# Optimization experiments

Hardware: AMD Instinct MI355X
Metric: run time of the kernel (lower is better)

Reference implementation:

```python
import jax, jax.numpy as jnp
import numpy as np

N_NODES = 50000
N_EDGES = 800000
IN_FEATS = 1024
LAYERS = [128, 128]
EPS = 1e-5  # BatchNorm1d eps


def setup_inputs() -> dict:
    key = jax.random.key(0)
    ks = jax.random.split(key, 24)
    inp = {}
    inp["in_feat"] = jax.random.normal(ks[0], (N_NODES, IN_FEATS), jnp.float32)
    inp["src"] = jax.random.randint(ks[1], (N_EDGES,), 0, N_NODES, dtype=jnp.int32)
    inp["dst"] = jax.random.randint(ks[2], (N_EDGES,), 0, N_NODES, dtype=jnp.int32)
    dims = [IN_FEATS] + LAYERS
    i = 3
    for l in range(len(LAYERS)):
        din, dout = dims[l], dims[l + 1]
        s = 1.0 / np.sqrt(din)
        inp[f"W{l}"] = jax.random.uniform(ks[i], (din, dout), jnp.float32, -s, s); i += 1
        inp[f"b{l}"] = jnp.zeros((dout,), jnp.float32)
        inp[f"Wr{l}"] = jax.random.uniform(ks[i], (din, dout), jnp.float32, -s, s); i += 1
        inp[f"br{l}"] = jnp.zeros((dout,), jnp.float32)
        inp[f"gamma{l}"] = jnp.ones((dout,), jnp.float32)
        inp[f"beta{l}"] = jnp.zeros((dout,), jnp.float32)
        inp[f"mean{l}"] = jnp.zeros((dout,), jnp.float32)
        inp[f"var{l}"] = jnp.ones((dout,), jnp.float32)
    s = 1.0 / np.sqrt(LAYERS[-1])
    inp["Wd"] = jax.random.uniform(ks[i], (LAYERS[-1], 2), jnp.float32, -s, s)
    inp["bd"] = jnp.zeros((2,), jnp.float32)
    return inp


def gcn_layer(h, src, dst, W, b, Wr, br, gamma, beta, mean, var):
    # dgllife GCNLayer: GraphConv(norm='none', activation=relu) -> residual -> dropout(id, eval) -> BN(eval)
    msg = (h @ W)[src]                                        # [E, dout] gather of transformed src feats
    agg = jax.ops.segment_sum(msg, dst, num_segments=N_NODES)  # scatter-add to dst nodes
    new = jax.nn.relu(agg + b)                                 # GraphConv bias + activation
    res = jax.nn.relu(h @ Wr + br)                             # residual Linear + activation
    new = new + res
    return (new - mean) * jax.lax.rsqrt(var + EPS) * gamma + beta  # BatchNorm1d eval


def reference(in_feat, src, dst,
              W0, b0, Wr0, br0, gamma0, beta0, mean0, var0,
              W1, b1, Wr1, br1, gamma1, beta1, mean1, var1,
              Wd, bd):
    h = gcn_layer(in_feat, src, dst, W0, b0, Wr0, br0, gamma0, beta0, mean0, var0)
    h = gcn_layer(h, src, dst, W1, b1, Wr1, br1, gamma1, beta1, mean1, var1)
    logits = h @ Wd + bd                                       # [N, 2]
    return jax.nn.softmax(logits, axis=1)
```

## Files before the change

### kernel.cpp

```cpp
#include <hip/hip_runtime.h>
#include <math.h>

#define NNODES 50000
#define NEDGES 800000
#define KIN 1024
#define DH 128

typedef __bf16 bf16x8 __attribute__((ext_vector_type(8)));
typedef float floatx4 __attribute__((ext_vector_type(4)));

__global__ void k_zero2(int* __restrict__ a, int* __restrict__ b, int n) {
  int i = blockIdx.x * blockDim.x + threadIdx.x;
  if (i < n) { a[i] = 0; b[i] = 0; }
}

__global__ void k_hist(const int* __restrict__ dst, int* __restrict__ cnt, int E) {
  int i = blockIdx.x * blockDim.x + threadIdx.x;
  if (i < E) atomicAdd(&cnt[dst[i]], 1);
}

__global__ __launch_bounds__(1024) void k_scan_local(const int* __restrict__ cnt,
                                                     int* __restrict__ row_ptr,
                                                     int* __restrict__ bsum, int n) {
  __shared__ int sd[1024];
  int t = threadIdx.x;
  int i = blockIdx.x * 1024 + t;
  int v = (i < n) ? cnt[i] : 0;
  sd[t] = v;
  __syncthreads();
  for (int off = 1; off < 1024; off <<= 1) {
    int tv = (t >= off) ? sd[t - off] : 0;
    __syncthreads();
    sd[t] += tv;
    __syncthreads();
  }
  if (i < n) row_ptr[i] = sd[t] - v;
  if (t == 1023) bsum[blockIdx.x] = sd[t];
}

__global__ void k_scan_sums(const int* __restrict__ bsum, int* __restrict__ boff,
                            int nb, int* __restrict__ row_ptr, int n) {
  int lane = threadIdx.x;
  int v = (lane < nb) ? bsum[lane] : 0;
  int incl = v;
  for (int off = 1; off < 64; off <<= 1) {
    int t = __shfl_up(incl, off);
    if (lane >= off) incl += t;
  }
  boff[lane] = incl - v;
  if (lane == 63) row_ptr[n] = incl;
}

__global__ void k_scan_add(int* __restrict__ row_ptr, const int* __restrict__ boff, int n) {
  int i = blockIdx.x * blockDim.x + threadIdx.x;
  if (i < n) row_ptr[i] += boff[i >> 10];
}

__global__ void k_fill(const int* __restrict__ src, const int* __restrict__ dst,
                       const int* __restrict__ row_ptr, int* __restrict__ cursor,
                       int* __restrict__ csr_src, int E) {
  int i = blockIdx.x * blockDim.x + threadIdx.x;
  if (i < E) {
    int d = dst[i];
    int pos = row_ptr[d] + atomicAdd(&cursor[d], 1);
    csr_src[pos] = src[i];
  }
}

__global__ __launch_bounds__(256) void k_prepB(const float* __restrict__ W,
                                               const float* __restrict__ Wr,
                                               __bf16* __restrict__ Bt, int K, int kbits) {
  int id = blockIdx.x * 256 + threadIdx.x;
  int k = id & (K - 1);
  int n = id >> kbits;
  float v = (n < DH) ? W[(size_t)k * DH + n] : Wr[(size_t)k * DH + (n - DH)];
  Bt[(size_t)n * K + k] = (__bf16)v;
}

__device__ __forceinline__ void load_lds16(const void* g, void* l) {
  __builtin_amdgcn_global_load_lds(
      (const __attribute__((address_space(1))) unsigned int*)g,
      (__attribute__((address_space(3))) unsigned int*)l, 16, 0, 0);
}

template <typename AT, int K>
__global__ __launch_bounds__(256, 4) void k_gemm_mfma(
    const AT* __restrict__ X, const __bf16* __restrict__ Bt,
    const float* __restrict__ br, __bf16* __restrict__ XW,
    float* __restrict__ RES, int M) {
  __shared__ alignas(16) __bf16 As[32 * 72];
  __shared__ alignas(16) __bf16 Bs[256 * 64];
  const int tid = threadIdx.x;
  const int lane = tid & 63;
  const int w = tid >> 6;
  const int l15 = lane & 15;
  const int quad = lane >> 4;
  const int bm0 = blockIdx.x * 32;

  const int arow = tid >> 3;
  const int akq = (tid & 7) << 3;
  int agrow = bm0 + arow; if (agrow > M - 1) agrow = M - 1;
  const AT* aptr = X + (size_t)agrow * K + akq;

  floatx4 acc[2][4];
#pragma unroll
  for (int i = 0; i < 2; ++i)
#pragma unroll
    for (int j = 0; j < 4; ++j) acc[i][j] = (floatx4)0.f;

  for (int k0 = 0; k0 < K; k0 += 64) {
    if constexpr (sizeof(AT) == 4) {
      const float4 u = *(const float4*)(aptr + k0);
      const float4 v = *(const float4*)(aptr + k0 + 4);
      bf16x8 h;
      h[0] = (__bf16)u.x; h[1] = (__bf16)u.y; h[2] = (__bf16)u.z; h[3] = (__bf16)u.w;
      h[4] = (__bf16)v.x; h[5] = (__bf16)v.y; h[6] = (__bf16)v.z; h[7] = (__bf16)v.w;
      *(bf16x8*)&As[arow * 72 + akq] = h;
    } else {
      *(bf16x8*)&As[arow * 72 + akq] = *(const bf16x8*)(aptr + k0);
    }
#pragma unroll
    for (int ii = 0; ii < 8; ++ii) {
      const int wi = ii * 4 + w;
      const int n = wi * 8 + (lane >> 3);
      const int c = lane & 7;
      const int cs = c ^ (n & 7);
      const char* g = (const char*)Bt + (size_t)n * (K * 2) + (size_t)k0 * 2 + cs * 16;
      load_lds16(g, (char*)Bs + wi * 1024);
    }
    __syncthreads();
    bf16x8 af[2][2], bfr[4][2];
#pragma unroll
    for (int mt = 0; mt < 2; ++mt)
#pragma unroll
      for (int ks = 0; ks < 2; ++ks)
        af[mt][ks] = *(const bf16x8*)&As[(mt * 16 + l15) * 72 + ks * 32 + quad * 8];
#pragma unroll
    for (int nt = 0; nt < 4; ++nt) {
      const int n = w * 64 + nt * 16 + l15;
#pragma unroll
      for (int ks = 0; ks < 2; ++ks) {
        const int ch = (ks * 4 + quad) ^ (n & 7);
        bfr[nt][ks] = *(const bf16x8*)&Bs[n * 64 + ch * 8];
      }
    }
#pragma unroll
    for (int ks = 0; ks < 2; ++ks)
#pragma unroll
      for (int mt = 0; mt < 2; ++mt)
#pragma unroll
        for (int nt = 0; nt < 4; ++nt)
          acc[mt][nt] = __builtin_amdgcn_mfma_f32_16x16x32_bf16(af[mt][ks], bfr[nt][ks],
                                                                acc[mt][nt], 0, 0, 0);
    __syncthreads();
  }

  float* Cb = (float*)Bs;
#pragma unroll
  for (int mt = 0; mt < 2; ++mt)
#pragma unroll
    for (int nt = 0; nt < 4; ++nt)
#pragma unroll
      for (int r = 0; r < 4; ++r)
        Cb[(mt * 16 + quad * 4 + r) * 256 + (w * 64 + nt * 16 + l15)] = acc[mt][nt][r];
  __syncthreads();
  const int row = tid >> 3;
  const int seg = tid & 7;
  const int grow = bm0 + row;
  if (grow < M) {
    if (seg < 4) {
      const int c0 = seg * 32;
#pragma unroll
      for (int j = 0; j < 4; ++j) {
        const float4 v0 = *(const float4*)&Cb[row * 256 + c0 + j * 8];
        const float4 v1 = *(const float4*)&Cb[row * 256 + c0 + j * 8 + 4];
        bf16x8 h;
        h[0] = (__bf16)v0.x; h[1] = (__bf16)v0.y; h[2] = (__bf16)v0.z; h[3] = (__bf16)v0.w;
        h[4] = (__bf16)v1.x; h[5] = (__bf16)v1.y; h[6] = (__bf16)v1.z; h[7] = (__bf16)v1.w;
        *(bf16x8*)&XW[(size_t)grow * DH + c0 + j * 8] = h;
      }
    } else {
      const int c0 = (seg - 4) * 32;
#pragma unroll
      for (int j = 0; j < 8; ++j) {
        const float4 v = *(const float4*)&Cb[row * 256 + 128 + c0 + j * 4];
        const float4 bb = *(const float4*)&br[c0 + j * 4];
        *(float4*)&RES[(size_t)grow * DH + c0 + j * 4] =
            make_float4(fmaxf(v.x + bb.x, 0.f), fmaxf(v.y + bb.y, 0.f),
                        fmaxf(v.z + bb.z, 0.f), fmaxf(v.w + bb.w, 0.f));
      }
    }
  }
}

template <int MODE>
__global__ __launch_bounds__(256) void k_agg2(
    const __bf16* __restrict__ XW, const float* __restrict__ RES,
    const int* __restrict__ row_ptr, const int* __restrict__ csr_src,
    const float* __restrict__ b, const float* __restrict__ gamma,
    const float* __restrict__ beta, const float* __restrict__ mean,
    const float* __restrict__ var, const float* __restrict__ Wd,
    const float* __restrict__ bd, void* __restrict__ hout, int M) {
  const int node = (blockIdx.x << 2) + (threadIdx.x >> 6);
  const int lane = threadIdx.x & 63;
  if (node >= M) return;
  const int s = row_ptr[node], e = row_ptr[node + 1];
  const unsigned* xw = (const unsigned*)XW;
  float ax = 0.f, ay = 0.f;
  int i = s;
  for (; i + 3 < e; i += 4) {
    const int s0 = csr_src[i], s1 = csr_src[i + 1], s2 = csr_src[i + 2], s3 = csr_src[i + 3];
    const unsigned u0 = xw[(size_t)s0 * 64 + lane];
    const unsigned u1 = xw[(size_t)s1 * 64 + lane];
    const unsigned u2 = xw[(size_t)s2 * 64 + lane];
    const unsigned u3 = xw[(size_t)s3 * 64 + lane];
    ax += __uint_as_float(u0 << 16) + __uint_as_float(u1 << 16) +
          __uint_as_float(u2 << 16) + __uint_as_float(u3 << 16);
    ay += __uint_as_float(u0 & 0xffff0000u) + __uint_as_float(u1 & 0xffff0000u) +
          __uint_as_float(u2 & 0xffff0000u) + __uint_as_float(u3 & 0xffff0000u);
  }
  for (; i < e; ++i) {
    const unsigned u = xw[(size_t)csr_src[i] * 64 + lane];
    ax += __uint_as_float(u << 16);
    ay += __uint_as_float(u & 0xffff0000u);
  }
  const int f0 = lane << 1;
  const float2 bb = *(const float2*)&b[f0];
  const float2 rr = *(const float2*)&RES[(size_t)node * DH + f0];
  const float2 mm = *(const float2*)&mean[f0];
  const float2 vv = *(const float2*)&var[f0];
  const float2 gg = *(const float2*)&gamma[f0];
  const float2 be = *(const float2*)&beta[f0];
  const float x0 = fmaxf(ax + bb.x, 0.f) + rr.x;
  const float x1 = fmaxf(ay + bb.y, 0.f) + rr.y;
  const float y0 = (x0 - mm.x) * rsqrtf(vv.x + 1e-5f) * gg.x + be.x;
  const float y1 = (x1 - mm.y) * rsqrtf(vv.y + 1e-5f) * gg.y + be.y;
  if (MODE == 0) {
    union { __bf16 h[2]; unsigned u; } pk;
    pk.h[0] = (__bf16)y0;
    pk.h[1] = (__bf16)y1;
    ((unsigned*)hout)[(size_t)node * 64 + lane] = pk.u;
  } else {
    const float4 wv = *(const float4*)&Wd[f0 * 2];
    float l0 = y0 * wv.x + y1 * wv.z;
    float l1 = y0 * wv.y + y1 * wv.w;
#pragma unroll
    for (int off = 32; off > 0; off >>= 1) {
      l0 += __shfl_down(l0, off);
      l1 += __shfl_down(l1, off);
    }
    if (lane == 0) {
      l0 += bd[0];
      l1 += bd[1];
      const float m = fmaxf(l0, l1);
      const float e0 = expf(l0 - m), e1 = expf(l1 - m);
      const float inv = 1.f / (e0 + e1);
      float* out = (float*)hout;
      out[(size_t)node * 2] = e0 * inv;
      out[(size_t)node * 2 + 1] = e1 * inv;
    }
  }
}

extern "C" void kernel_launch(void* const* d_in, const int* in_sizes, int n_in,
                              void* d_out, int out_size, void* d_ws, size_t ws_size,
                              hipStream_t stream) {
  const float* in_feat = (const float*)d_in[0];
  const int* src = (const int*)d_in[1];
  const int* dst = (const int*)d_in[2];
  const float* W0 = (const float*)d_in[3];
  const float* b0 = (const float*)d_in[4];
  const float* Wr0 = (const float*)d_in[5];
  const float* br0 = (const float*)d_in[6];
  const float* gamma0 = (const float*)d_in[7];
  const float* beta0 = (const float*)d_in[8];
  const float* mean0 = (const float*)d_in[9];
  const float* var0 = (const float*)d_in[10];
  const float* W1 = (const float*)d_in[11];
  const float* b1 = (const float*)d_in[12];
  const float* Wr1 = (const float*)d_in[13];
  const float* br1 = (const float*)d_in[14];
  const float* gamma1 = (const float*)d_in[15];
  const float* beta1 = (const float*)d_in[16];
  const float* mean1 = (const float*)d_in[17];
  const float* var1 = (const float*)d_in[18];
  const float* Wd = (const float*)d_in[19];
  const float* bd = (const float*)d_in[20];
  float* out = (float*)d_out;

  char* ws = (char*)d_ws;
  size_t off = 0;
  auto alloc = [&](size_t bytes) {
    void* p = ws + off;
    off += (bytes + 255) & ~(size_t)255;
    return p;
  };
  __bf16* XWb = (__bf16*)alloc(sizeof(__bf16) * (size_t)NNODES * DH);
  __bf16* h1 = (__bf16*)alloc(sizeof(__bf16) * (size_t)NNODES * DH);
  float* RES = (float*)alloc(sizeof(float) * (size_t)NNODES * DH);
  int* cnt = (int*)alloc(sizeof(int) * NNODES);
  int* cursor = (int*)alloc(sizeof(int) * NNODES);
  int* row_ptr = (int*)alloc(sizeof(int) * (NNODES + 1));
  int* csr_src = (int*)alloc(sizeof(int) * NEDGES);
  int* bsum = (int*)alloc(sizeof(int) * 64);
  int* boff = (int*)alloc(sizeof(int) * 64);
  __bf16* Bt0 = (__bf16*)alloc(sizeof(__bf16) * 256 * KIN);
  __bf16* Bt1 = (__bf16*)alloc(sizeof(__bf16) * 256 * DH);

  const int nb = (NNODES + 1023) / 1024;
  k_zero2<<<(NNODES + 255) / 256, 256, 0, stream>>>(cnt, cursor, NNODES);
  k_hist<<<(NEDGES + 255) / 256, 256, 0, stream>>>(dst, cnt, NEDGES);
  k_scan_local<<<nb, 1024, 0, stream>>>(cnt, row_ptr, bsum, NNODES);
  k_scan_sums<<<1, 64, 0, stream>>>(bsum, boff, nb, row_ptr, NNODES);
  k_scan_add<<<(NNODES + 255) / 256, 256, 0, stream>>>(row_ptr, boff, NNODES);
  k_fill<<<(NEDGES + 255) / 256, 256, 0, stream>>>(src, dst, row_ptr, cursor, csr_src, NEDGES);

  k_prepB<<<KIN, 256, 0, stream>>>(W0, Wr0, Bt0, KIN, 10);
  k_prepB<<<DH, 256, 0, stream>>>(W1, Wr1, Bt1, DH, 7);

  const int ggrid = (NNODES + 31) / 32;
  const int agrid = (NNODES + 3) / 4;
  k_gemm_mfma<float, KIN><<<ggrid, 256, 0, stream>>>(in_feat, Bt0, br0, XWb, RES, NNODES);
  k_agg2<0><<<agrid, 256, 0, stream>>>(XWb, RES, row_ptr, csr_src, b0, gamma0, beta0,
                                       mean0, var0, nullptr, nullptr, h1, NNODES);
  k_gemm_mfma<__bf16, DH><<<ggrid, 256, 0, stream>>>(h1, Bt1, br1, XWb, RES, NNODES);
  k_agg2<1><<<agrid, 256, 0, stream>>>(XWb, RES, row_ptr, csr_src, b1, gamma1, beta1,
                                       mean1, var1, Wd, bd, out, NNODES);
}
```

Before: 556.2 us.

## Pre-pack weights in MFMA fragment order and stage full A tile in LDS

Weights are now packed once into the exact per-lane MFMA B-fragment layout, so the GEMM reads B straight from global/L2 into registers with coalesced 16-byte loads instead of staging it through LDS every k-step. The whole 32xK A tile is loaded and converted to bf16 in one pass into a swizzled LDS buffer, which removes the per-iteration syncthreads from the main loop. The cost is 64KB of LDS per block for K=1024, which limits occupancy, and B traffic now relies on the cache for reuse across blocks.

```diff
diff --git a/kernel.cpp b/kernel.cpp
--- a/kernel.cpp
+++ b/kernel.cpp
@@ -67,29 +67,35 @@
   }
 }
 
-__global__ __launch_bounds__(256) void k_prepB(const float* __restrict__ W,
+__global__ __launch_bounds__(256) void k_prepF(const float* __restrict__ W,
                                                const float* __restrict__ Wr,
-                                               __bf16* __restrict__ Bt, int K, int kbits) {
-  int id = blockIdx.x * 256 + threadIdx.x;
-  int k = id & (K - 1);
-  int n = id >> kbits;
-  float v = (n < DH) ? W[(size_t)k * DH + n] : Wr[(size_t)k * DH + (n - DH)];
-  Bt[(size_t)n * K + k] = (__bf16)v;
-}
-
-__device__ __forceinline__ void load_lds16(const void* g, void* l) {
-  __builtin_amdgcn_global_load_lds(
-      (const __attribute__((address_space(1))) unsigned int*)g,
-      (__attribute__((address_space(3))) unsigned int*)l, 16, 0, 0);
+                                               __bf16* __restrict__ Bf) {
+  const int id = blockIdx.x * 256 + threadIdx.x;
+  const int lane = id & 63;
+  const int ks = (id >> 6) & 1;
+  const int nt = (id >> 7) & 15;
+  const int kb = id >> 11;
+  const int n = nt * 16 + (lane & 15);
+  const int k0 = kb * 64 + ks * 32 + (lane >> 4) * 8;
+  bf16x8 h;
+#pragma unroll
+  for (int j = 0; j < 8; ++j) {
+    const int k = k0 + j;
+    const float v = (n < DH) ? W[(size_t)k * DH + n] : Wr[(size_t)k * DH + (n - DH)];
+    h[j] = (__bf16)v;
+  }
+  *(bf16x8*)&Bf[(size_t)id * 8] = h;
 }
 
 template <typename AT, int K>
-__global__ __launch_bounds__(256, 4) void k_gemm_mfma(
-    const AT* __restrict__ X, const __bf16* __restrict__ Bt,
+__global__ __launch_bounds__(256) void k_gemm3(
+    const AT* __restrict__ X, const __bf16* __restrict__ Bf,
     const float* __restrict__ br, __bf16* __restrict__ XW,
     float* __restrict__ RES, int M) {
-  __shared__ alignas(16) __bf16 As[32 * 72];
-  __shared__ alignas(16) __bf16 Bs[256 * 64];
+  constexpr unsigned ABYTES = 32u * K * 2u;
+  constexpr unsigned SMEM = (ABYTES > 32768u) ? ABYTES : 32768u;
+  __shared__ alignas(16) char smem[SMEM];
+  __bf16* As = (__bf16*)smem;
   const int tid = threadIdx.x;
   const int lane = tid & 63;
   const int w = tid >> 6;
@@ -97,10 +103,28 @@
   const int quad = lane >> 4;
   const int bm0 = blockIdx.x * 32;
 
-  const int arow = tid >> 3;
-  const int akq = (tid & 7) << 3;
-  int agrow = bm0 + arow; if (agrow > M - 1) agrow = M - 1;
-  const AT* aptr = X + (size_t)agrow * K + akq;
+  {
+    const int row = tid >> 3;
+    int grow = bm0 + row;
+    if (grow > M - 1) grow = M - 1;
+    const AT* ap = X + (size_t)grow * K;
+#pragma unroll 4
+    for (int j = 0; j < K / 64; ++j) {
+      const int c = (tid & 7) + 8 * j;
+      bf16x8 h;
+      if constexpr (sizeof(AT) == 4) {
+        const float4 u = *(const float4*)(ap + c * 8);
+        const float4 v = *(const float4*)(ap + c * 8 + 4);
+        h[0] = (__bf16)u.x; h[1] = (__bf16)u.y; h[2] = (__bf16)u.z; h[3] = (__bf16)u.w;
+        h[4] = (__bf16)v.x; h[5] = (__bf16)v.y; h[6] = (__bf16)v.z; h[7] = (__bf16)v.w;
+      } else {
+        h = *(const bf16x8*)(ap + c * 8);
+      }
+      const int cs = (c & ~7) | ((c ^ row) & 7);
+      *(bf16x8*)&As[(size_t)row * K + (cs << 3)] = h;
+    }
+  }
+  __syncthreads();
 
   floatx4 acc[2][4];
 #pragma unroll
@@ -108,42 +132,27 @@
 #pragma unroll
     for (int j = 0; j < 4; ++j) acc[i][j] = (floatx4)0.f;
 
-  for (int k0 = 0; k0 < K; k0 += 64) {
-    if constexpr (sizeof(AT) == 4) {
-      const float4 u = *(const float4*)(aptr + k0);
-      const float4 v = *(const float4*)(aptr + k0 + 4);
-      bf16x8 h;
-      h[0] = (__bf16)u.x; h[1] = (__bf16)u.y; h[2] = (__bf16)u.z; h[3] = (__bf16)u.w;
-      h[4] = (__bf16)v.x; h[5] = (__bf16)v.y; h[6] = (__bf16)v.z; h[7] = (__bf16)v.w;
-      *(bf16x8*)&As[arow * 72 + akq] = h;
-    } else {
-      *(bf16x8*)&As[arow * 72 + akq] = *(const bf16x8*)(aptr + k0);
-    }
-#pragma unroll
-    for (int ii = 0; ii < 8; ++ii) {
-      const int wi = ii * 4 + w;
-      const int n = wi * 8 + (lane >> 3);
-      const int c = lane & 7;
-      const int cs = c ^ (n & 7);
-      const char* g = (const char*)Bt + (size_t)n * (K * 2) + (size_t)k0 * 2 + cs * 16;
-      load_lds16(g, (char*)Bs + wi * 1024);
-    }
-    __syncthreads();
-    bf16x8 af[2][2], bfr[4][2];
+#pragma unroll 2
+  for (int kb = 0; kb < K / 64; ++kb) {
+    bf16x8 bfr[4][2];
+#pragma unroll
+    for (int nt = 0; nt < 4; ++nt)
+#pragma unroll
+      for (int ks = 0; ks < 2; ++ks) {
+        const int ntg = (w << 2) + nt;
+        const size_t idx = ((((size_t)kb * 16 + ntg) * 2 + ks) * 64 + lane) * 8;
+        bfr[nt][ks] = *(const bf16x8*)(Bf + idx);
+      }
+    bf16x8 af[2][2];
 #pragma unroll
     for (int mt = 0; mt < 2; ++mt)
 #pragma unroll
-      for (int ks = 0; ks < 2; ++ks)
-        af[mt][ks] = *(const bf16x8*)&As[(mt * 16 + l15) * 72 + ks * 32 + quad * 8];
-#pragma unroll
-    for (int nt = 0; nt < 4; ++nt) {
-      const int n = w * 64 + nt * 16 + l15;
-#pragma unroll
       for (int ks = 0; ks < 2; ++ks) {
-        const int ch = (ks * 4 + quad) ^ (n & 7);
-        bfr[nt][ks] = *(const bf16x8*)&Bs[n * 64 + ch * 8];
-      }
-    }
+        const int row = mt * 16 + l15;
+        const int c = kb * 8 + ks * 4 + quad;
+        const int cs = (c & ~7) | ((c ^ row) & 7);
+        af[mt][ks] = *(const bf16x8*)&As[(size_t)row * K + (cs << 3)];
+      }
 #pragma unroll
     for (int ks = 0; ks < 2; ++ks)
 #pragma unroll
@@ -152,17 +161,17 @@
         for (int nt = 0; nt < 4; ++nt)
           acc[mt][nt] = __builtin_amdgcn_mfma_f32_16x16x32_bf16(af[mt][ks], bfr[nt][ks],
                                                                 acc[mt][nt], 0, 0, 0);
-    __syncthreads();
-  }
-
-  float* Cb = (float*)Bs;
+  }
+
+  __syncthreads();
+  float* Cb = (float*)smem;
 #pragma unroll
   for (int mt = 0; mt < 2; ++mt)
 #pragma unroll
     for (int nt = 0; nt < 4; ++nt)
 #pragma unroll
       for (int r = 0; r < 4; ++r)
-        Cb[(mt * 16 + quad * 4 + r) * 256 + (w * 64 + nt * 16 + l15)] = acc[mt][nt][r];
+        Cb[(mt * 16 + quad * 4 + r) * 256 + ((w << 6) + nt * 16 + l15)] = acc[mt][nt][r];
   __syncthreads();
   const int row = tid >> 3;
   const int seg = tid & 7;
@@ -304,8 +313,8 @@
   int* csr_src = (int*)alloc(sizeof(int) * NEDGES);
   int* bsum = (int*)alloc(sizeof(int) * 64);
   int* boff = (int*)alloc(sizeof(int) * 64);
-  __bf16* Bt0 = (__bf16*)alloc(sizeof(__bf16) * 256 * KIN);
-  __bf16* Bt1 = (__bf16*)alloc(sizeof(__bf16) * 256 * DH);
+  __bf16* Bf0 = (__bf16*)alloc(sizeof(__bf16) * 256 * KIN);
+  __bf16* Bf1 = (__bf16*)alloc(sizeof(__bf16) * 256 * DH);
 
   const int nb = (NNODES + 1023) / 1024;
   k_zero2<<<(NNODES + 255) / 256, 256, 0, stream>>>(cnt, cursor, NNODES);
@@ -315,15 +324,15 @@
   k_scan_add<<<(NNODES + 255) / 256, 256, 0, stream>>>(row_ptr, boff, NNODES);
   k_fill<<<(NEDGES + 255) / 256, 256, 0, stream>>>(src, dst, row_ptr, cursor, csr_src, NEDGES);
 
-  k_prepB<<<KIN, 256, 0, stream>>>(W0, Wr0, Bt0, KIN, 10);
-  k_prepB<<<DH, 256, 0, stream>>>(W1, Wr1, Bt1, DH, 7);
+  k_prepF<<<(KIN / 64) * 16 * 2 * 64 / 256, 256, 0, stream>>>(W0, Wr0, Bf0);
+  k_prepF<<<(DH / 64) * 16 * 2 * 64 / 256, 256, 0, stream>>>(W1, Wr1, Bf1);
 
   const int ggrid = (NNODES + 31) / 32;
   const int agrid = (NNODES + 3) / 4;
-  k_gemm_mfma<float, KIN><<<ggrid, 256, 0, stream>>>(in_feat, Bt0, br0, XWb, RES, NNODES);
+  k_gemm3<float, KIN><<<ggrid, 256, 0, stream>>>(in_feat, Bf0, br0, XWb, RES, NNODES);
   k_agg2<0><<<agrid, 256, 0, stream>>>(XWb, RES, row_ptr, csr_src, b0, gamma0, beta0,
                                        mean0, var0, nullptr, nullptr, h1, NNODES);
-  k_gemm_mfma<__bf16, DH><<<ggrid, 256, 0, stream>>>(h1, Bt1, br1, XWb, RES, NNODES);
+  k_gemm3<__bf16, DH><<<ggrid, 256, 0, stream>>>(h1, Bf1, br1, XWb, RES, NNODES);
   k_agg2<1><<<agrid, 256, 0, stream>>>(XWb, RES, row_ptr, csr_src, b1, gamma1, beta1,
                                        mean1, var1, Wd, bd, out, NNODES);
 }
```

New measurement: 567.8 us. 2.1% more time.
